# Optimization experiments

Hardware: AMD Instinct MI355X
Metric: run time of the kernel (lower is better)

Reference implementation:

```python
import math
import jax, jax.numpy as jnp
import numpy as np

W_SIZE = 7
NUM_HEADS = 12


def _shift_masks(w: int, d: int):
    # upper/lower mask (applied to last row of windows)
    ul = np.zeros((w * w, w * w), np.float32)
    ul[-d * w:, :-d * w] = -np.inf
    ul[:-d * w, -d * w:] = -np.inf
    # left/right mask (applied to last column of windows)
    lr = np.zeros((w, w, w, w), np.float32)
    lr[:, -d:, :, :-d] = -np.inf
    lr[:, :-d, :, -d:] = -np.inf
    lr = lr.reshape(w * w, w * w)
    return jnp.asarray(ul), jnp.asarray(lr)


def _rel_pos_index(w: int):
    # standard Swin relative-position index, shape (w*w, w*w), values in [0, (2w-1)^2)
    coords = np.stack(np.meshgrid(np.arange(w), np.arange(w), indexing='ij'), 0).reshape(2, -1)  # (2, w*w)
    rel = coords[:, :, None] - coords[:, None, :]  # (2, ww, ww)
    idx = (rel[0] + w - 1) * (2 * w - 1) + (rel[1] + w - 1)
    return jnp.asarray(idx, dtype=jnp.int32)


def setup_inputs() -> dict:
    key = jax.random.key(0)
    ks = jax.random.split(key, 6)
    E, w = 384, W_SIZE
    return {
        'x': jax.random.normal(ks[0], (32, 56, 56, E), jnp.float32),
        'w_qkv': jax.random.normal(ks[1], (3 * E, E), jnp.float32) * 0.02,
        'b_qkv': jax.random.normal(ks[2], (3 * E,), jnp.float32) * 0.02,
        'w_proj': jax.random.normal(ks[3], (E, E), jnp.float32) * 0.02,
        'b_proj': jax.random.normal(ks[4], (E,), jnp.float32) * 0.02,
        'rel_table': jax.random.normal(ks[5], ((2 * w - 1) ** 2, NUM_HEADS), jnp.float32) * 0.02,
    }


def reference(x, w_qkv, b_qkv, w_proj, b_proj, rel_table):
    w = W_SIZE
    heads = NUM_HEADS
    B, H, Wd, C = x.shape
    hd = C // heads
    nh, nw, ww = H // w, Wd // w, w * w

    # shift (matches torch roll(shifts=(-w//2, -w//2)) == -4 for w=7)
    x = jnp.roll(x, ((-w) // 2, (-w) // 2), axis=(1, 2))

    # window partition: (B, nh, nw, ww, C)
    xw = x.reshape(B, nh, w, nw, w, C).transpose(0, 1, 3, 2, 4, 5).reshape(B, nh, nw, ww, C)

    qkv = xw @ w_qkv.T + b_qkv  # (B, nh, nw, ww, 3C)
    q, k, v = jnp.split(qkv, 3, axis=-1)

    def heads_first(t):  # (B, nh, nw, heads, ww, hd)
        return t.reshape(B, nh, nw, ww, heads, hd).transpose(0, 1, 2, 4, 3, 5)

    q, k, v = heads_first(q), heads_first(k), heads_first(v)

    attn = jnp.einsum('bhwnqd,bhwnkd->bhwnqk', q, k) * (1.0 / math.sqrt(hd))

    # relative position bias: (heads, ww, ww)
    bias = rel_table[_rel_pos_index(w)].transpose(2, 0, 1)
    attn = attn + bias

    # shift masks on last row / last column of windows
    ul, lr = _shift_masks(w, w // 2)
    mask = jnp.zeros((nh, nw, 1, ww, ww), attn.dtype)
    mask = mask.at[-1].add(ul)
    mask = mask.at[:, -1].add(lr)
    attn = attn + mask

    p = jax.nn.softmax(attn, axis=-1)
    o = jnp.einsum('bhwnqk,bhwnkd->bhwnqd', p, v)  # (B, nh, nw, heads, ww, hd)

    # merge heads and un-window
    o = o.transpose(0, 1, 2, 4, 3, 5).reshape(B, nh, nw, w, w, C)
    o = o.transpose(0, 1, 3, 2, 4, 5).reshape(B, H, Wd, C)

    o = jnp.roll(o, (w // 2, w // 2), axis=(1, 2))
    return o @ w_proj.T + b_proj
```

## Files before the change

### kernel.cpp

```cpp
#include <hip/hip_runtime.h>
#include <hip/hip_bf16.h>


typedef __bf16 bf16x8 __attribute__((ext_vector_type(8)));
typedef float  floatx4 __attribute__((ext_vector_type(4)));
typedef short  short8  __attribute__((ext_vector_type(8)));
typedef unsigned long long u64;

#define MFMA16(a, b, c) __builtin_amdgcn_mfma_f32_16x16x32_bf16((a), (b), (c), 0, 0, 0)

static __device__ __forceinline__ void gload_lds16(const void* g, void* l) {
  __builtin_amdgcn_global_load_lds(
      (const __attribute__((address_space(1))) void*)g,
      (__attribute__((address_space(3))) void*)l, 16, 0, 0);
}

static __device__ __forceinline__ int src_off(int gm) {
  int win = gm / 49, t = gm - win * 49;
  int b = win >> 6, rr = win & 63;
  int wi = rr >> 3, wj = rr & 7;
  int ty = t / 7, tx = t - ty * 7;
  int y = wi * 7 + ty + 4; if (y >= 56) y -= 56;
  int x = wj * 7 + tx + 4; if (x >= 56) x -= 56;
  return ((b * 56 + y) * 56 + x) * 384;
}

static __device__ __forceinline__ int dst_off(int gm) {
  int win = gm / 49, t = gm - win * 49;
  int b = win >> 6, rr = win & 63;
  int wi = rr >> 3, wj = rr & 7;
  int ty = t / 7, tx = t - ty * 7;
  int y = wi * 7 + ty + 3; if (y >= 56) y -= 56;
  int x = wj * 7 + tx + 3; if (x >= 56) x -= 56;
  return ((b * 56 + y) * 56 + x) * 384;
}

static __device__ __forceinline__ float bf_lo(unsigned u) {
  union { unsigned v; float f; } c; c.v = u << 16; return c.f;
}
static __device__ __forceinline__ float bf_hi(unsigned u) {
  union { unsigned v; float f; } c; c.v = u & 0xFFFF0000u; return c.f;
}

__global__ __launch_bounds__(256) void prep_kernel(
    const float* __restrict__ w_qkv, const float* __restrict__ w_proj,
    const float* __restrict__ rel_table,
    __hip_bfloat16* __restrict__ wqkv_bf, __hip_bfloat16* __restrict__ wproj_bf,
    __hip_bfloat16* __restrict__ bias2) {
  const int N1 = 3 * 384 * 384;
  const int N2 = 384 * 384;
  const int N3 = 12 * 4 * 4 * 64 * 4;
  int i = blockIdx.x * 256 + threadIdx.x;
  if (i < N1) wqkv_bf[i] = __float2bfloat16(w_qkv[i]);
  int j = i - N1;
  if (j >= 0 && j < N2) wproj_bf[j] = __float2bfloat16(w_proj[j]);
  int k = i - N1 - N2;
  if (k >= 0 && k < N3) {
    int r = k & 3;
    int lp = (k >> 2) & 63;
    int ni = (k >> 8) & 3;
    int mi = (k >> 10) & 3;
    int head = k >> 12;
    int m = mi * 16 + (lp & 15);
    int n = ni * 16 + (lp >> 4) * 4 + r;
    float val = -1e30f;
    if (m < 49 && n < 49) {
      int dy = m / 7 - n / 7 + 6;
      int dx = m % 7 - n % 7 + 6;
      val = rel_table[(dy * 13 + dx) * 12 + head];
    }
    bias2[k] = __float2bfloat16(val);
  }
}

__global__ __launch_bounds__(256) void xconv_kernel(
    const float* __restrict__ x, __hip_bfloat16* __restrict__ xw) {
  int gid = blockIdx.x * 256 + threadIdx.x;
  int row = gid / 48;
  int c = (gid - row * 48) * 8;
  int so = src_off(row) + c;
  floatx4 a = *(const floatx4*)(x + so);
  floatx4 b = *(const floatx4*)(x + so + 4);
  union { __hip_bfloat16 h[8]; short8 s; } u;
#pragma unroll
  for (int i = 0; i < 4; ++i) {
    u.h[i]     = __float2bfloat16(a[i]);
    u.h[4 + i] = __float2bfloat16(b[i]);
  }
  *(short8*)(xw + (size_t)row * 384 + c) = u.s;
}

__global__ __launch_bounds__(256) void qkv_kernel(
    const __hip_bfloat16* __restrict__ xw, const __hip_bfloat16* __restrict__ wq,
    const float* __restrict__ bqkv,
    __hip_bfloat16* __restrict__ qb, __hip_bfloat16* __restrict__ kb,
    __hip_bfloat16* __restrict__ vt) {
  __shared__ __hip_bfloat16 lds[2 * 16384];
  int blk = blockIdx.x;
  int b2 = (blk & 7) * 882 + (blk >> 3);
  int mt = b2 / 9, nt = b2 - mt * 9;
  int tid = threadIdx.x;
  int l = tid & 63, wv = tid >> 6;
  int wm = wv >> 1, wn = wv & 1;
  int g = l >> 4, q16 = l & 15;

  const bool swapped = (nt >= 6);
  const int aro = (swapped ? wn : wm) * 64;
  const int bro = (swapped ? wm : wn) * 64;

  int sr = tid >> 3;
  int sc = tid & 7;
  int scs = sc ^ (sr & 7);

  const __hip_bfloat16* abase = xw + (size_t)(mt * 128) * 384;
  const __hip_bfloat16* bbase = wq + (size_t)(nt * 128) * 384;

  floatx4 acc[4][4];
#pragma unroll
  for (int i = 0; i < 4; ++i)
#pragma unroll
    for (int j = 0; j < 4; ++j)
#pragma unroll
      for (int r = 0; r < 4; ++r) acc[i][j][r] = 0.f;

  auto stage = [&](int buf, int kt) {
    int k0 = kt * 64;
    __hip_bfloat16* la = lds + buf * 16384;
#pragma unroll
    for (int c = 0; c < 4; ++c) {
      int r = c * 32 + sr;
      gload_lds16(abase + (size_t)r * 384 + k0 + scs * 8, la + c * 2048 + tid * 8);
      gload_lds16(bbase + (size_t)r * 384 + k0 + scs * 8, la + 8192 + c * 2048 + tid * 8);
    }
  };

  auto compute = [&](int buf) {
    const __hip_bfloat16* la = lds + buf * 16384;
    const __hip_bfloat16* lb = la + 8192;
#pragma unroll
    for (int kk = 0; kk < 2; ++kk) {
      bf16x8 af[4], bf[4];
#pragma unroll
      for (int i = 0; i < 4; ++i) {
        int r = aro + i * 16 + q16;
        int cp = (kk * 4 + g) ^ (r & 7);
        af[i] = *(const bf16x8*)(la + r * 64 + cp * 8);
      }
#pragma unroll
      for (int i = 0; i < 4; ++i) {
        int r = bro + i * 16 + q16;
        int cp = (kk * 4 + g) ^ (r & 7);
        bf[i] = *(const bf16x8*)(lb + r * 64 + cp * 8);
      }
      if (!swapped) {
#pragma unroll
        for (int i = 0; i < 4; ++i)
#pragma unroll
          for (int j = 0; j < 4; ++j)
            acc[i][j] = MFMA16(af[i], bf[j], acc[i][j]);
      } else {
#pragma unroll
        for (int i = 0; i < 4; ++i)
#pragma unroll
          for (int j = 0; j < 4; ++j)
            acc[i][j] = MFMA16(bf[i], af[j], acc[i][j]);
      }
    }
  };

  stage(0, 0);
  stage(1, 1);
#pragma unroll
  for (int t = 0; t < 6; ++t) {
    if (t < 5) asm volatile("s_waitcnt vmcnt(8)" ::: "memory");
    else       asm volatile("s_waitcnt vmcnt(0)" ::: "memory");
    __builtin_amdgcn_s_barrier();
    __builtin_amdgcn_sched_barrier(0);
    compute(t & 1);
    if (t < 4) {
      __builtin_amdgcn_s_barrier();
      stage(t & 1, t + 2);
    }
  }

  if (!swapped) {
    const bool isq = (nt < 3);
    __hip_bfloat16* ob2 = isq ? qb : kb;
#pragma unroll
    for (int ni = 0; ni < 4; ++ni) {
      int n = nt * 128 + wn * 64 + ni * 16 + q16;
      float bn = bqkv[n];
      int nn = isq ? n : (n - 384);
#pragma unroll
      for (int mi = 0; mi < 4; ++mi) {
#pragma unroll
        for (int r = 0; r < 4; ++r) {
          int gm = mt * 128 + wm * 64 + mi * 16 + g * 4 + r;
          float v = acc[mi][ni][r] + bn;
          if (isq) v *= 0.17677669529663687f;
          ob2[gm * 384 + nn] = __float2bfloat16(v);
        }
      }
    }
  } else {
    int win4[4], t4[4];
#pragma unroll
    for (int bj = 0; bj < 4; ++bj) {
      int gm = mt * 128 + wn * 64 + bj * 16 + q16;
      int w = gm / 49;
      win4[bj] = w;
      t4[bj] = gm - w * 49;
    }
#pragma unroll
    for (int ai = 0; ai < 4; ++ai) {
#pragma unroll
      for (int r = 0; r < 4; ++r) {
        int n = nt * 128 + wm * 64 + ai * 16 + g * 4 + r;
        float bn = bqkv[n];
        int nnv = n - 768;
#pragma unroll
        for (int bj = 0; bj < 4; ++bj) {
          vt[((size_t)win4[bj] * 384 + nnv) * 64 + t4[bj]] =
              __float2bfloat16(acc[ai][bj][r] + bn);
        }
      }
    }
  }
}

__global__ __launch_bounds__(256, 4) void attnproj_kernel(
    const __hip_bfloat16* __restrict__ qb, const __hip_bfloat16* __restrict__ kb,
    const __hip_bfloat16* __restrict__ vt, const __hip_bfloat16* __restrict__ bias2,
    const __hip_bfloat16* __restrict__ wp, const float* __restrict__ bproj,
    float* __restrict__ out) {
  __shared__ __hip_bfloat16 o_lds[49][392];
  int blk = blockIdx.x;
  int win = (blk & 7) * 256 + (blk >> 3);
  int tid = threadIdx.x;
  int wv = tid >> 6, l = tid & 63;
  int g = l >> 4, q16 = l & 15;
  int wr = win & 63;
  const bool lastrow = ((wr >> 3) == 7);
  const bool lastcol = ((wr & 7) == 7);

  unsigned long long badbits = 0ull;
  if (lastrow || lastcol) {
#pragma unroll
    for (int mi = 0; mi < 4; ++mi) {
      int m = mi * 16 + q16;
      int m7 = m % 7;
      bool m28 = (m >= 28), m74 = (m7 >= 4);
#pragma unroll
      for (int ni = 0; ni < 4; ++ni) {
#pragma unroll
        for (int r = 0; r < 4; ++r) {
          int n = ni * 16 + g * 4 + r;
          bool bad = (lastrow && (m28 != (n >= 28))) ||
                     (lastcol && (m74 != ((n % 7) >= 4)));
          if (bad) badbits |= (1ull << (mi * 16 + ni * 4 + r));
        }
      }
    }
  }

  floatx4 zc;
  zc[0] = zc[1] = zc[2] = zc[3] = 0.f;

#pragma unroll 1
  for (int hh = 0; hh < 3; ++hh) {
    int head = wv * 3 + hh;
    const __hip_bfloat16* qp = qb + (size_t)(win * 49) * 384 + head * 32 + g * 8;
    const __hip_bfloat16* kp = kb + (size_t)(win * 49) * 384 + head * 32 + g * 8;

    bf16x8 bk[4];
#pragma unroll
    for (int ni = 0; ni < 4; ++ni) {
      int row = ni * 16 + q16;
      row = row < 49 ? row : 48;
      bk[ni] = *(const bf16x8*)(kp + row * 384);
    }
    const __hip_bfloat16* vp = vt + ((size_t)win * 384 + head * 32) * 64;
    bf16x8 va[2][2];
#pragma unroll
    for (int ai = 0; ai < 2; ++ai)
#pragma unroll
      for (int ks = 0; ks < 2; ++ks)
        va[ai][ks] = *(const bf16x8*)(vp + (ai * 16 + q16) * 64 + ks * 32 + g * 8);

    const __hip_bfloat16* b2 = bias2 + (size_t)head * 4096;

#pragma unroll
    for (int mi = 0; mi < 4; ++mi) {
      int arow = mi * 16 + q16;
      arow = arow < 49 ? arow : 48;
      bf16x8 aqm = *(const bf16x8*)(qp + arow * 384);

      floatx4 stm[4];
      __builtin_amdgcn_s_setprio(1);
#pragma unroll
      for (int ni = 0; ni < 4; ++ni)
        stm[ni] = MFMA16(bk[ni], aqm, zc);
      __builtin_amdgcn_s_setprio(0);

      uint2 braw[4];
#pragma unroll
      for (int ni = 0; ni < 4; ++ni)
        braw[ni] = *(const uint2*)(b2 + ((mi * 4 + ni) * 64 + l) * 4);

      float vals[4][4];
      float mx = -1e30f;
#pragma unroll
      for (int ni = 0; ni < 4; ++ni) {
#pragma unroll
        for (int r = 0; r < 4; ++r) {
          float bb = (r == 0) ? bf_lo(braw[ni].x) : (r == 1) ? bf_hi(braw[ni].x)
                     : (r == 2) ? bf_lo(braw[ni].y) : bf_hi(braw[ni].y);
          float v = stm[ni][r] + bb;
          if ((badbits >> (mi * 16 + ni * 4 + r)) & 1) v = -1e30f;
          vals[ni][r] = v;
          mx = fmaxf(mx, v);
        }
      }
      mx = fmaxf(mx, __shfl_xor(mx, 16));
      mx = fmaxf(mx, __shfl_xor(mx, 32));
      float sum = 0.f;
#pragma unroll
      for (int ni = 0; ni < 4; ++ni) {
#pragma unroll
        for (int r = 0; r < 4; ++r) {
          float p = __expf(vals[ni][r] - mx);
          vals[ni][r] = p;
          sum += p;
        }
      }
      sum += __shfl_xor(sum, 16);
      sum += __shfl_xor(sum, 32);
      float inv = 1.0f / sum;

      u64 pk4[4];
#pragma unroll
      for (int ni = 0; ni < 4; ++ni) {
        union { __hip_bfloat16 h[4]; u64 u; } pk;
#pragma unroll
        for (int r = 0; r < 4; ++r) pk.h[r] = __float2bfloat16(vals[ni][r] * inv);
        pk4[ni] = pk.u;
      }

      bf16x8 bp[2];
#pragma unroll
      for (int ks = 0; ks < 2; ++ks) {
        u64 A  = pk4[2 * ks];
        u64 A3 = pk4[2 * ks + 1];
        u64 B16 = __shfl_xor(A, 16);
        u64 B32 = __shfl_xor(A, 32);
        u64 B48 = __shfl_xor(A, 48);
        u64 C16 = __shfl_xor(A3, 16);
        u64 C32 = __shfl_xor(A3, 32);
        u64 C48 = __shfl_xor(A3, 48);
        u64 lo = (g == 0) ? A : (g == 1) ? B48 : (g == 2) ? C32 : C16;
        u64 hi = (g == 0) ? B16 : (g == 1) ? B32 : (g == 2) ? C48 : A3;
        union { u64 w[2]; bf16x8 v; } cb;
        cb.w[0] = lo; cb.w[1] = hi;
        bp[ks] = cb.v;
      }

      floatx4 o2[2];
      o2[0] = o2[1] = zc;
      __builtin_amdgcn_s_setprio(1);
#pragma unroll
      for (int ai = 0; ai < 2; ++ai)
#pragma unroll
        for (int ks = 0; ks < 2; ++ks)
          o2[ai] = MFMA16(va[ai][ks], bp[ks], o2[ai]);
      __builtin_amdgcn_s_setprio(0);

      int m = mi * 16 + q16;
      if (m < 49) {
#pragma unroll
        for (int ai = 0; ai < 2; ++ai)
#pragma unroll
          for (int r = 0; r < 4; ++r)
            o_lds[m][head * 32 + ai * 16 + g * 4 + r] = __float2bfloat16(o2[ai][r]);
      }
    }
  }

  __syncthreads();

#pragma unroll 1
  for (int pass = 0; pass < 2; ++pass) {
    int n0 = wv * 96 + pass * 48;
    floatx4 pacc[4][3];
#pragma unroll
    for (int i = 0; i < 4; ++i)
#pragma unroll
      for (int j = 0; j < 3; ++j) pacc[i][j] = zc;

#pragma unroll
    for (int kk = 0; kk < 12; ++kk) {
      int k0 = kk * 32;
      bf16x8 af[4], bfr[3];
#pragma unroll
      for (int mi = 0; mi < 4; ++mi) {
        int row = mi * 16 + q16;
        row = row < 49 ? row : 48;
        af[mi] = *(const bf16x8*)&o_lds[row][k0 + g * 8];
      }
#pragma unroll
      for (int ni = 0; ni < 3; ++ni)
        bfr[ni] = *(const bf16x8*)(wp + (size_t)(n0 + ni * 16 + q16) * 384 + k0 + g * 8);
      __builtin_amdgcn_s_setprio(1);
#pragma unroll
      for (int mi = 0; mi < 4; ++mi)
#pragma unroll
        for (int ni = 0; ni < 3; ++ni)
          pacc[mi][ni] = MFMA16(af[mi], bfr[ni], pacc[mi][ni]);
      __builtin_amdgcn_s_setprio(0);
    }

#pragma unroll
    for (int mi = 0; mi < 4; ++mi) {
#pragma unroll
      for (int r = 0; r < 4; ++r) {
        int m = mi * 16 + g * 4 + r;
        if (m < 49) {
          int off = dst_off(win * 49 + m);
#pragma unroll
          for (int ni = 0; ni < 3; ++ni) {
            int n = n0 + ni * 16 + q16;
            out[off + n] = pacc[mi][ni][r] + bproj[n];
          }
        }
      }
    }
  }
}

extern "C" void kernel_launch(void* const* d_in, const int* in_sizes, int n_in,
                              void* d_out, int out_size, void* d_ws, size_t ws_size,
                              hipStream_t stream) {
  const float* x         = (const float*)d_in[0];
  const float* w_qkv     = (const float*)d_in[1];
  const float* b_qkv     = (const float*)d_in[2];
  const float* w_proj    = (const float*)d_in[3];
  const float* b_proj    = (const float*)d_in[4];
  const float* rel_table = (const float*)d_in[5];
  float* out = (float*)d_out;

  char* ws = (char*)d_ws;
  const size_t OFF_WQKV  = 0;
  const size_t OFF_WPROJ = 884736;
  const size_t OFF_BIAS2 = 1179648;
  const size_t OFF_Q     = 1572864;
  const size_t OFF_K     = OFF_Q + 77070336;
  const size_t OFF_VT    = OFF_K + 77070336;

  __hip_bfloat16* wqkv_bf  = (__hip_bfloat16*)(ws + OFF_WQKV);
  __hip_bfloat16* wproj_bf = (__hip_bfloat16*)(ws + OFF_WPROJ);
  __hip_bfloat16* bias2    = (__hip_bfloat16*)(ws + OFF_BIAS2);
  __hip_bfloat16* qb       = (__hip_bfloat16*)(ws + OFF_Q);
  __hip_bfloat16* kb       = (__hip_bfloat16*)(ws + OFF_K);
  __hip_bfloat16* vt       = (__hip_bfloat16*)(ws + OFF_VT);
  __hip_bfloat16* xw       = (__hip_bfloat16*)d_out;


  prep_kernel<<<3072, 256, 0, stream>>>(w_qkv, w_proj, rel_table, wqkv_bf, wproj_bf, bias2);
  xconv_kernel<<<18816, 256, 0, stream>>>(x, xw);
  qkv_kernel<<<7056, 256, 0, stream>>>(xw, wqkv_bf, b_qkv, qb, kb, vt);
  attnproj_kernel<<<2048, 256, 0, stream>>>(qb, kb, vt, bias2, wproj_bf, b_proj, out);
}
```

Measured before the change: 379.1 us.

## Load QKV weight fragments directly from global memory, halving LDS use

The QKV GEMM kernel no longer stages the weight tile in LDS. Each wave reads its B fragments directly from global memory (cache-resident weights), which halves the shared-memory footprint and allows launch_bounds(256,4) to raise occupancy. The pipeline is reworked into a simpler double-buffered prefetch with __syncthreads, and MFMA sections are wrapped in s_setprio. The risk is that global loads of B now sit on the critical path, each fragment is re-read by several waves without LDS reuse, and the fine-grained vmcnt-based overlap is lost.

```diff
diff --git a/kernel.cpp b/kernel.cpp
--- a/kernel.cpp
+++ b/kernel.cpp
@@ -90,12 +90,12 @@
   *(short8*)(xw + (size_t)row * 384 + c) = u.s;
 }
 
-__global__ __launch_bounds__(256) void qkv_kernel(
+__global__ __launch_bounds__(256, 4) void qkv_kernel(
     const __hip_bfloat16* __restrict__ xw, const __hip_bfloat16* __restrict__ wq,
     const float* __restrict__ bqkv,
     __hip_bfloat16* __restrict__ qb, __hip_bfloat16* __restrict__ kb,
     __hip_bfloat16* __restrict__ vt) {
-  __shared__ __hip_bfloat16 lds[2 * 16384];
+  __shared__ __hip_bfloat16 lds[2 * 8192];
   int blk = blockIdx.x;
   int b2 = (blk & 7) * 882 + (blk >> 3);
   int mt = b2 / 9, nt = b2 - mt * 9;
@@ -125,20 +125,19 @@
 
   auto stage = [&](int buf, int kt) {
     int k0 = kt * 64;
-    __hip_bfloat16* la = lds + buf * 16384;
+    __hip_bfloat16* la = lds + buf * 8192;
 #pragma unroll
     for (int c = 0; c < 4; ++c) {
       int r = c * 32 + sr;
       gload_lds16(abase + (size_t)r * 384 + k0 + scs * 8, la + c * 2048 + tid * 8);
-      gload_lds16(bbase + (size_t)r * 384 + k0 + scs * 8, la + 8192 + c * 2048 + tid * 8);
     }
   };
 
-  auto compute = [&](int buf) {
-    const __hip_bfloat16* la = lds + buf * 16384;
-    const __hip_bfloat16* lb = la + 8192;
+  auto compute = [&](int buf, int kt) {
+    const __hip_bfloat16* la = lds + buf * 8192;
 #pragma unroll
     for (int kk = 0; kk < 2; ++kk) {
+      int kg = kt * 64 + kk * 32;
       bf16x8 af[4], bf[4];
 #pragma unroll
       for (int i = 0; i < 4; ++i) {
@@ -147,11 +146,9 @@
         af[i] = *(const bf16x8*)(la + r * 64 + cp * 8);
       }
 #pragma unroll
-      for (int i = 0; i < 4; ++i) {
-        int r = bro + i * 16 + q16;
-        int cp = (kk * 4 + g) ^ (r & 7);
-        bf[i] = *(const bf16x8*)(lb + r * 64 + cp * 8);
-      }
+      for (int i = 0; i < 4; ++i)
+        bf[i] = *(const bf16x8*)(bbase + (size_t)(bro + i * 16 + q16) * 384 + kg + g * 8);
+      __builtin_amdgcn_s_setprio(1);
       if (!swapped) {
 #pragma unroll
         for (int i = 0; i < 4; ++i)
@@ -165,22 +162,17 @@
           for (int j = 0; j < 4; ++j)
             acc[i][j] = MFMA16(bf[i], af[j], acc[i][j]);
       }
+      __builtin_amdgcn_s_setprio(0);
     }
   };
 
   stage(0, 0);
-  stage(1, 1);
+  __syncthreads();
 #pragma unroll
   for (int t = 0; t < 6; ++t) {
-    if (t < 5) asm volatile("s_waitcnt vmcnt(8)" ::: "memory");
-    else       asm volatile("s_waitcnt vmcnt(0)" ::: "memory");
-    __builtin_amdgcn_s_barrier();
-    __builtin_amdgcn_sched_barrier(0);
-    compute(t & 1);
-    if (t < 4) {
-      __builtin_amdgcn_s_barrier();
-      stage(t & 1, t + 2);
-    }
+    if (t < 5) stage((t + 1) & 1, t + 1);
+    compute(t & 1, t);
+    __syncthreads();
   }
 
   if (!swapped) {
```

Measured after the change: 979.0 us. +158.2%, slower.
